# Performance work log

Measured on AMD Instinct MI355X. Metric: run time of the kernel, lower is better.

## Reference

```python
import jax, jax.numpy as jnp
import numpy as np

B, LD, LP, DIM = 8, 128, 1000, 128
LN_EPS = 1e-5


def layer_norm(x, gamma, beta, eps=LN_EPS):
    mu = jnp.mean(x, axis=-1, keepdims=True)
    var = jnp.mean(jnp.square(x - mu), axis=-1, keepdims=True)
    return (x - mu) * jax.lax.rsqrt(var + eps) * gamma + beta


def setup_inputs() -> dict:
    key = jax.random.key(0)
    ks = jax.random.split(key, 8)
    s = 1.0 / np.sqrt(DIM)
    return {
        "drug_conv": jax.random.normal(ks[0], (B, LD, DIM), dtype=jnp.float32),
        "protein_conv": jax.random.normal(ks[1], (B, LP, DIM), dtype=jnp.float32),
        "W_d": jax.random.normal(ks[2], (DIM, DIM), dtype=jnp.float32) * s,
        "b_d": jnp.zeros((DIM,), dtype=jnp.float32),
        "W_p": jax.random.normal(ks[3], (DIM, DIM), dtype=jnp.float32) * s,
        "b_p": jnp.zeros((DIM,), dtype=jnp.float32),
        "W_att": jax.random.normal(ks[4], (DIM, DIM), dtype=jnp.float32) * s,
        "b_att": jnp.zeros((DIM,), dtype=jnp.float32),
        "gamma1": jnp.ones((DIM,), dtype=jnp.float32),
        "beta1": jnp.zeros((DIM,), dtype=jnp.float32),
        "gamma2": jnp.ones((DIM,), dtype=jnp.float32),
        "beta2": jnp.zeros((DIM,), dtype=jnp.float32),
    }


def reference(drug_conv, protein_conv, W_d, b_d, W_p, b_p, W_att, b_att,
              gamma1, beta1, gamma2, beta2):
    # drug_conv: (B, LD, DIM), protein_conv: (B, LP, DIM)
    d_att = drug_conv @ W_d.T + b_d        # (B, LD, DIM)
    p_att = protein_conv @ W_p.T + b_p     # (B, LP, DIM)
    # Pairwise additive interaction (B, LD, LP, DIM) -- the fusable hotspot.
    M = jax.nn.relu(d_att[:, :, None, :] + p_att[:, None, :, :])
    # Linear commutes with mean: apply attention_layer after reduction.
    compound_att = jax.nn.sigmoid(jnp.mean(M, axis=2) @ W_att.T + b_att)  # (B, LD, DIM)
    protein_att = jax.nn.sigmoid(jnp.mean(M, axis=1) @ W_att.T + b_att)   # (B, LP, DIM)
    drug = drug_conv * 0.5 + drug_conv * compound_att
    prot = protein_conv * 0.5 + protein_conv * protein_att
    # MaxPool1d over full length axis == max over L, then LayerNorm(dim).
    drug_vec = layer_norm(jnp.max(drug, axis=1), gamma1, beta1)   # (B, DIM)
    prot_vec = layer_norm(jnp.max(prot, axis=1), gamma2, beta2)   # (B, DIM)
    return (drug_vec, prot_vec)
```

## Files before the change

kernel.cpp:

```cpp
#include <hip/hip_runtime.h>
#include <math.h>

#define B 8
#define LD 128
#define LP 1000
#define LP_PAD 1008
#define DIM 128
#define R 8
#define LN_EPS 1e-5f

#define NBLK_D (B * LD / R)
#define NBLK_P (B * LP / R)
#define SEG_D (NBLK_D / B)
#define SEG_P (NBLK_P / B)

__global__ __launch_bounds__(DIM) void gemv_both(
        const float* __restrict__ Xd, const float* __restrict__ Xp,
        const float* __restrict__ Wd, const float* __restrict__ bd,
        const float* __restrict__ Wp, const float* __restrict__ bp,
        float* __restrict__ outd, float* __restrict__ outp) {
    const int blk = blockIdx.x;
    const int t = threadIdx.x;

    const float *X, *W, *bias;
    float* out;
    int row0;
    if (blk < NBLK_D) { X = Xd; W = Wd; bias = bd; out = outd; row0 = blk * R; }
    else              { X = Xp; W = Wp; bias = bp; out = outp; row0 = (blk - NBLK_D) * R; }

    __shared__ float4 xs4[R][DIM / 4];
    {
        const float4* Xv = reinterpret_cast<const float4*>(X + (size_t)row0 * DIM);
        float4* s = (float4*)xs4;
        s[t] = Xv[t];
        s[t + DIM] = Xv[t + DIM];
    }
    __syncthreads();

    float acc[R];
    const float bv = bias[t];
#pragma unroll
    for (int r = 0; r < R; ++r) acc[r] = bv;

    const float4* w4 = reinterpret_cast<const float4*>(W + t * DIM);
#pragma unroll
    for (int k = 0; k < DIM / 4; ++k) {
        const float4 w = w4[k];
#pragma unroll
        for (int r = 0; r < R; ++r) {
            const float4 x = xs4[r][k];
            acc[r] += w.x * x.x + w.y * x.y + w.z * x.z + w.w * x.w;
        }
    }
#pragma unroll
    for (int r = 0; r < R; ++r) out[(row0 + r) * DIM + t] = acc[r];
}

__global__ __launch_bounds__(256) void pairwise(
        const float* __restrict__ d_att, const float* __restrict__ p_att,
        float* __restrict__ Mc, float* __restrict__ Mp) {
    const int blk = blockIdx.x;
    const int b = blk >> 7;
    const int d = blk & (DIM - 1);
    const int t = threadIdx.x;

    __shared__ float xs[LD];
    __shared__ float2 ys2[LP_PAD / 2];
    __shared__ float red[LD * 8];

    if (t < LD) xs[t] = d_att[(b * LD + t) * DIM + d];
    for (int j = t; j < LP_PAD; j += 256) {
        ((float*)ys2)[j] = (j < LP) ? p_att[(b * LP + j) * DIM + d] : -1e30f;
    }
    __syncthreads();

    for (int p = t; p < LP_PAD / 2; p += 256) {
        const float2 y = ys2[p];
        float2 acc = make_float2(0.f, 0.f);
#pragma unroll 8
        for (int i = 0; i < LD; ++i) {
            const float x = xs[i];
            acc.x += fmaxf(0.f, x + y.x);
            acc.y += fmaxf(0.f, x + y.y);
        }
        const int j = 2 * p;
        if (j < LP)     Mp[(b * LP + j) * DIM + d]     = acc.x * (1.f / (float)LD);
        if (j + 1 < LP) Mp[(b * LP + j + 1) * DIM + d] = acc.y * (1.f / (float)LD);
    }

    {
        const int rq = t >> 3;
        const int sl = t & 7;
        const float x0 = xs[4 * rq + 0];
        const float x1 = xs[4 * rq + 1];
        const float x2 = xs[4 * rq + 2];
        const float x3 = xs[4 * rq + 3];
        float2 a0 = make_float2(0.f, 0.f), a1 = a0, a2 = a0, a3 = a0;
        for (int p = sl; p < LP_PAD / 2; p += 8) {
            const float2 y = ys2[p];
            a0.x += fmaxf(0.f, x0 + y.x); a0.y += fmaxf(0.f, x0 + y.y);
            a1.x += fmaxf(0.f, x1 + y.x); a1.y += fmaxf(0.f, x1 + y.y);
            a2.x += fmaxf(0.f, x2 + y.x); a2.y += fmaxf(0.f, x2 + y.y);
            a3.x += fmaxf(0.f, x3 + y.x); a3.y += fmaxf(0.f, x3 + y.y);
        }
        red[(4 * rq + 0) * 8 + sl] = a0.x + a0.y;
        red[(4 * rq + 1) * 8 + sl] = a1.x + a1.y;
        red[(4 * rq + 2) * 8 + sl] = a2.x + a2.y;
        red[(4 * rq + 3) * 8 + sl] = a3.x + a3.y;
    }
    __syncthreads();
    if (t < LD) {
        float s = 0.f;
#pragma unroll
        for (int k = 0; k < 8; ++k) s += red[t * 8 + k];
        Mc[(b * LD + t) * DIM + d] = s * (1.f / (float)LP);
    }
}

__global__ __launch_bounds__(DIM) void gated_both(
        const float* __restrict__ Mc, const float* __restrict__ Mp,
        const float* __restrict__ W, const float* __restrict__ bias,
        const float* __restrict__ convd, const float* __restrict__ convp,
        float* __restrict__ pd, float* __restrict__ pp) {
    const int blk = blockIdx.x;
    const int t = threadIdx.x;

    const float *M, *conv;
    float* part;
    int row0;
    if (blk < NBLK_D) { M = Mc; conv = convd; part = pd + blk * DIM; row0 = blk * R; }
    else { const int pb = blk - NBLK_D; M = Mp; conv = convp; part = pp + pb * DIM; row0 = pb * R; }

    __shared__ float4 xs4[R][DIM / 4];
    {
        const float4* Mv = reinterpret_cast<const float4*>(M + (size_t)row0 * DIM);
        float4* s = (float4*)xs4;
        s[t] = Mv[t];
        s[t + DIM] = Mv[t + DIM];
    }
    __syncthreads();

    float acc[R];
    const float bv = bias[t];
#pragma unroll
    for (int r = 0; r < R; ++r) acc[r] = bv;

    const float4* w4 = reinterpret_cast<const float4*>(W + t * DIM);
#pragma unroll
    for (int k = 0; k < DIM / 4; ++k) {
        const float4 w = w4[k];
#pragma unroll
        for (int r = 0; r < R; ++r) {
            const float4 x = xs4[r][k];
            acc[r] += w.x * x.x + w.y * x.y + w.z * x.z + w.w * x.w;
        }
    }

    float m = -INFINITY;
#pragma unroll
    for (int r = 0; r < R; ++r) {
        const float att = 1.f / (1.f + expf(-acc[r]));
        const float v = conv[(row0 + r) * DIM + t] * (0.5f + att);
        m = fmaxf(m, v);
    }
    part[t] = m;
}

__global__ __launch_bounds__(256) void maxln_final(
        const float* __restrict__ pd, const float* __restrict__ pp,
        const float* __restrict__ gamma1, const float* __restrict__ beta1,
        const float* __restrict__ gamma2, const float* __restrict__ beta2,
        float* __restrict__ out) {
    const int blk = blockIdx.x;
    const int kind = blk >> 3;
    const int b = blk & 7;
    const int t = threadIdx.x & (DIM - 1);
    const int h = threadIdx.x >> 7;

    float m = -INFINITY;
    if (kind == 0) {
        const float* base = pd + b * SEG_D * DIM;
        for (int s = h; s < SEG_D; s += 2) m = fmaxf(m, base[s * DIM + t]);
    } else {
        const float* base = pp + b * SEG_P * DIM;
        for (int s = h; s < SEG_P; s += 2) m = fmaxf(m, base[s * DIM + t]);
    }

    __shared__ float sm[2][DIM];
    sm[h][t] = m;
    __syncthreads();

    __shared__ float s1[DIM];
    __shared__ float s2[DIM];
    if (threadIdx.x < DIM) {
        m = fmaxf(sm[0][t], sm[1][t]);
        sm[0][t] = m;
        s1[t] = m;
        s2[t] = m * m;
    }
    __syncthreads();
    for (int off = DIM / 2; off > 0; off >>= 1) {
        if (threadIdx.x < off) {
            s1[threadIdx.x] += s1[threadIdx.x + off];
            s2[threadIdx.x] += s2[threadIdx.x + off];
        }
        __syncthreads();
    }
    if (threadIdx.x < DIM) {
        const float mu = s1[0] * (1.f / (float)DIM);
        const float var = s2[0] * (1.f / (float)DIM) - mu * mu;
        const float inv = rsqrtf(var + LN_EPS);
        const float* gamma = kind ? gamma2 : gamma1;
        const float* beta  = kind ? beta2  : beta1;
        const float mv = sm[0][t];
        out[blk * DIM + t] = (mv - mu) * inv * gamma[t] + beta[t];
    }
}

extern "C" void kernel_launch(void* const* d_in, const int* in_sizes, int n_in,
                              void* d_out, int out_size, void* d_ws, size_t ws_size,
                              hipStream_t stream) {
    const float* drug_conv    = (const float*)d_in[0];
    const float* protein_conv = (const float*)d_in[1];
    const float* W_d   = (const float*)d_in[2];
    const float* b_d   = (const float*)d_in[3];
    const float* W_p   = (const float*)d_in[4];
    const float* b_p   = (const float*)d_in[5];
    const float* W_att = (const float*)d_in[6];
    const float* b_att = (const float*)d_in[7];
    const float* gamma1 = (const float*)d_in[8];
    const float* beta1  = (const float*)d_in[9];
    const float* gamma2 = (const float*)d_in[10];
    const float* beta2  = (const float*)d_in[11];
    float* out = (float*)d_out;

    float* ws = (float*)d_ws;
    const size_t n_datt = (size_t)B * LD * DIM;
    const size_t n_patt = (size_t)B * LP * DIM;
    float* d_att = ws;
    float* p_att = ws + n_datt;
    float* Mc    = ws + n_datt + n_patt;
    float* Mp    = ws + n_datt + n_patt + n_datt;
    float* pd = ws;
    float* pp = ws + (size_t)NBLK_D * DIM;

    gemv_both<<<NBLK_D + NBLK_P, DIM, 0, stream>>>(drug_conv, protein_conv,
                                                   W_d, b_d, W_p, b_p, d_att, p_att);
    pairwise<<<B * DIM, 256, 0, stream>>>(d_att, p_att, Mc, Mp);
    gated_both<<<NBLK_D + NBLK_P, DIM, 0, stream>>>(Mc, Mp, W_att, b_att,
                                                    drug_conv, protein_conv, pd, pp);
    maxln_final<<<16, 256, 0, stream>>>(pd, pp, gamma1, beta1, gamma2, beta2, out);
}
```

Before: 145.6 us.

## Use bf16 MFMA for input projections and gated attention linear

Replaces the scalar fp32 GEMV kernels for the drug/protein projections and the attention linear layer with bf16 MFMA 16x16x32 tiles, one wave per 16-row tile. A small kernel converts the three weight matrices to bf16 on each call, and the activation tiles are converted in registers. The gated kernel now does its partial max reduction per tile with lane shuffles and handles the ragged protein tail per batch. This lowers precision to bf16 for these matmuls, which may affect accuracy, and adds an extra launch for the weight conversion.

```diff
diff --git a/kernel.cpp b/kernel.cpp
--- a/kernel.cpp
+++ b/kernel.cpp
@@ -6,54 +6,81 @@
 #define LP 1000
 #define LP_PAD 1008
 #define DIM 128
-#define R 8
 #define LN_EPS 1e-5f
 
-#define NBLK_D (B * LD / R)
-#define NBLK_P (B * LP / R)
-#define SEG_D (NBLK_D / B)
-#define SEG_P (NBLK_P / B)
-
-__global__ __launch_bounds__(DIM) void gemv_both(
+#define TILES_D (B * LD / 16)
+#define TILES_P (B * LP / 16)
+#define GTILES_D 64
+#define GTILES_PB 63
+#define GTILES_P (8 * GTILES_PB)
+#define SEG_D 8
+#define SEG_P GTILES_PB
+
+typedef __attribute__((ext_vector_type(8))) short bf16x8;
+typedef __attribute__((ext_vector_type(4))) float f32x4;
+
+__device__ inline short f2bf(float f) {
+    union { float f; unsigned u; } v; v.f = f;
+    unsigned r = v.u + 0x7fffu + ((v.u >> 16) & 1u);
+    return (short)(r >> 16);
+}
+
+__device__ inline bf16x8 cvt8(float4 lo, float4 hi) {
+    bf16x8 r;
+    r[0] = f2bf(lo.x); r[1] = f2bf(lo.y); r[2] = f2bf(lo.z); r[3] = f2bf(lo.w);
+    r[4] = f2bf(hi.x); r[5] = f2bf(hi.y); r[6] = f2bf(hi.z); r[7] = f2bf(hi.w);
+    return r;
+}
+
+__global__ __launch_bounds__(256) void conv_w(const float* __restrict__ W0,
+                                              const float* __restrict__ W1,
+                                              const float* __restrict__ W2,
+                                              short* __restrict__ out) {
+    const int idx = blockIdx.x * 256 + threadIdx.x;
+    const float* src = idx < 16384 ? W0 : (idx < 32768 ? W1 : W2);
+    out[idx] = f2bf(src[idx & 16383]);
+}
+
+__global__ __launch_bounds__(256) void mfma_gemv(
         const float* __restrict__ Xd, const float* __restrict__ Xp,
-        const float* __restrict__ Wd, const float* __restrict__ bd,
-        const float* __restrict__ Wp, const float* __restrict__ bp,
+        const short* __restrict__ Wdb, const float* __restrict__ bd,
+        const short* __restrict__ Wpb, const float* __restrict__ bp,
         float* __restrict__ outd, float* __restrict__ outp) {
-    const int blk = blockIdx.x;
-    const int t = threadIdx.x;
-
-    const float *X, *W, *bias;
-    float* out;
-    int row0;
-    if (blk < NBLK_D) { X = Xd; W = Wd; bias = bd; out = outd; row0 = blk * R; }
-    else              { X = Xp; W = Wp; bias = bp; out = outp; row0 = (blk - NBLK_D) * R; }
-
-    __shared__ float4 xs4[R][DIM / 4];
+    const int wave = (blockIdx.x * 256 + threadIdx.x) >> 6;
+    const int lane = threadIdx.x & 63;
+
+    const float* X; const short* Wb; const float* bias; float* out; int m0;
+    if (wave < TILES_D) { X = Xd; Wb = Wdb; bias = bd; out = outd; m0 = wave * 16; }
+    else { X = Xp; Wb = Wpb; bias = bp; out = outp; m0 = (wave - TILES_D) * 16; }
+
+    const int arow = lane & 15;
+    const int kgrp = lane >> 4;
+
+    bf16x8 afrag[4];
     {
-        const float4* Xv = reinterpret_cast<const float4*>(X + (size_t)row0 * DIM);
-        float4* s = (float4*)xs4;
-        s[t] = Xv[t];
-        s[t + DIM] = Xv[t + DIM];
-    }
-    __syncthreads();
-
-    float acc[R];
-    const float bv = bias[t];
-#pragma unroll
-    for (int r = 0; r < R; ++r) acc[r] = bv;
-
-    const float4* w4 = reinterpret_cast<const float4*>(W + t * DIM);
-#pragma unroll
-    for (int k = 0; k < DIM / 4; ++k) {
-        const float4 w = w4[k];
-#pragma unroll
-        for (int r = 0; r < R; ++r) {
-            const float4 x = xs4[r][k];
-            acc[r] += w.x * x.x + w.y * x.y + w.z * x.z + w.w * x.w;
-        }
-    }
-#pragma unroll
-    for (int r = 0; r < R; ++r) out[(row0 + r) * DIM + t] = acc[r];
+        const float* xrow = X + (size_t)(m0 + arow) * DIM + kgrp * 8;
+#pragma unroll
+        for (int kk = 0; kk < 4; ++kk)
+            afrag[kk] = cvt8(*(const float4*)(xrow + kk * 32),
+                             *(const float4*)(xrow + kk * 32 + 4));
+    }
+
+    const int ocol = lane & 15;
+    const int orow = (lane >> 4) * 4;
+#pragma unroll
+    for (int nt = 0; nt < 8; ++nt) {
+        const short* wrow = Wb + (size_t)(nt * 16 + arow) * DIM + kgrp * 8;
+        f32x4 c = {0.f, 0.f, 0.f, 0.f};
+#pragma unroll
+        for (int kk = 0; kk < 4; ++kk) {
+            const bf16x8 bfrag = *(const bf16x8*)(wrow + kk * 32);
+            c = __builtin_amdgcn_mfma_f32_16x16x32_bf16(afrag[kk], bfrag, c, 0, 0, 0);
+        }
+        const float bv = bias[nt * 16 + ocol];
+#pragma unroll
+        for (int r = 0; r < 4; ++r)
+            out[(size_t)(m0 + orow + r) * DIM + nt * 16 + ocol] = c[r] + bv;
+    }
 }
 
 __global__ __launch_bounds__(256) void pairwise(
@@ -117,53 +144,70 @@
     }
 }
 
-__global__ __launch_bounds__(DIM) void gated_both(
+__global__ __launch_bounds__(256) void mfma_gated(
         const float* __restrict__ Mc, const float* __restrict__ Mp,
-        const float* __restrict__ W, const float* __restrict__ bias,
+        const short* __restrict__ Wb, const float* __restrict__ bias,
         const float* __restrict__ convd, const float* __restrict__ convp,
         float* __restrict__ pd, float* __restrict__ pp) {
-    const int blk = blockIdx.x;
-    const int t = threadIdx.x;
-
-    const float *M, *conv;
-    float* part;
-    int row0;
-    if (blk < NBLK_D) { M = Mc; conv = convd; part = pd + blk * DIM; row0 = blk * R; }
-    else { const int pb = blk - NBLK_D; M = Mp; conv = convp; part = pp + pb * DIM; row0 = pb * R; }
-
-    __shared__ float4 xs4[R][DIM / 4];
-    {
-        const float4* Mv = reinterpret_cast<const float4*>(M + (size_t)row0 * DIM);
-        float4* s = (float4*)xs4;
-        s[t] = Mv[t];
-        s[t + DIM] = Mv[t + DIM];
-    }
-    __syncthreads();
-
-    float acc[R];
-    const float bv = bias[t];
-#pragma unroll
-    for (int r = 0; r < R; ++r) acc[r] = bv;
-
-    const float4* w4 = reinterpret_cast<const float4*>(W + t * DIM);
-#pragma unroll
-    for (int k = 0; k < DIM / 4; ++k) {
-        const float4 w = w4[k];
-#pragma unroll
-        for (int r = 0; r < R; ++r) {
-            const float4 x = xs4[r][k];
-            acc[r] += w.x * x.x + w.y * x.y + w.z * x.z + w.w * x.w;
-        }
-    }
-
-    float m = -INFINITY;
-#pragma unroll
-    for (int r = 0; r < R; ++r) {
-        const float att = 1.f / (1.f + expf(-acc[r]));
-        const float v = conv[(row0 + r) * DIM + t] * (0.5f + att);
-        m = fmaxf(m, v);
-    }
-    part[t] = m;
+    const int wave = (blockIdx.x * 256 + threadIdx.x) >> 6;
+    const int lane = threadIdx.x & 63;
+
+    const float* M; const float* conv; float* part; int m0; int valid;
+    if (wave < GTILES_D) {
+        M = Mc; conv = convd; part = pd + wave * DIM; m0 = wave * 16; valid = 16;
+    } else {
+        const int pb = wave - GTILES_D;
+        const int b = pb / GTILES_PB;
+        const int s = pb - b * GTILES_PB;
+        M = Mp; conv = convp; part = pp + pb * DIM;
+        m0 = b * LP + s * 16;
+        valid = (s * 16 + 16 <= LP) ? 16 : (LP - s * 16);
+    }
+
+    const int arow = lane & 15;
+    const int kgrp = lane >> 4;
+
+    bf16x8 afrag[4];
+    if (arow < valid) {
+        const float* mrow = M + (size_t)(m0 + arow) * DIM + kgrp * 8;
+#pragma unroll
+        for (int kk = 0; kk < 4; ++kk)
+            afrag[kk] = cvt8(*(const float4*)(mrow + kk * 32),
+                             *(const float4*)(mrow + kk * 32 + 4));
+    } else {
+        bf16x8 z;
+#pragma unroll
+        for (int j = 0; j < 8; ++j) z[j] = 0;
+#pragma unroll
+        for (int kk = 0; kk < 4; ++kk) afrag[kk] = z;
+    }
+
+    const int ocol = lane & 15;
+    const int orow = (lane >> 4) * 4;
+#pragma unroll
+    for (int nt = 0; nt < 8; ++nt) {
+        const short* wrow = Wb + (size_t)(nt * 16 + arow) * DIM + kgrp * 8;
+        f32x4 c = {0.f, 0.f, 0.f, 0.f};
+#pragma unroll
+        for (int kk = 0; kk < 4; ++kk) {
+            const bf16x8 bfrag = *(const bf16x8*)(wrow + kk * 32);
+            c = __builtin_amdgcn_mfma_f32_16x16x32_bf16(afrag[kk], bfrag, c, 0, 0, 0);
+        }
+        const float bv = bias[nt * 16 + ocol];
+        float m = -INFINITY;
+#pragma unroll
+        for (int r = 0; r < 4; ++r) {
+            const int rr = orow + r;
+            if (rr < valid) {
+                const float att = 1.f / (1.f + __expf(-(c[r] + bv)));
+                const float v = conv[(size_t)(m0 + rr) * DIM + nt * 16 + ocol] * (0.5f + att);
+                m = fmaxf(m, v);
+            }
+        }
+        m = fmaxf(m, __shfl_xor(m, 16));
+        m = fmaxf(m, __shfl_xor(m, 32));
+        if (lane < 16) part[nt * 16 + lane] = m;
+    }
 }
 
 __global__ __launch_bounds__(256) void maxln_final(
@@ -212,8 +256,7 @@
         const float inv = rsqrtf(var + LN_EPS);
         const float* gamma = kind ? gamma2 : gamma1;
         const float* beta  = kind ? beta2  : beta1;
-        const float mv = sm[0][t];
-        out[blk * DIM + t] = (mv - mu) * inv * gamma[t] + beta[t];
+        out[blk * DIM + t] = (sm[0][t] - mu) * inv * gamma[t] + beta[t];
     }
 }
 
@@ -241,13 +284,18 @@
     float* p_att = ws + n_datt;
     float* Mc    = ws + n_datt + n_patt;
     float* Mp    = ws + n_datt + n_patt + n_datt;
+    short* wbf   = (short*)(ws + 2310144);
+    short* wb_d   = wbf;
+    short* wb_p   = wbf + 16384;
+    short* wb_att = wbf + 32768;
     float* pd = ws;
-    float* pp = ws + (size_t)NBLK_D * DIM;
-
-    gemv_both<<<NBLK_D + NBLK_P, DIM, 0, stream>>>(drug_conv, protein_conv,
-                                                   W_d, b_d, W_p, b_p, d_att, p_att);
+    float* pp = ws + GTILES_D * DIM;
+
+    conv_w<<<192, 256, 0, stream>>>(W_d, W_p, W_att, wbf);
+    mfma_gemv<<<(TILES_D + TILES_P) / 4, 256, 0, stream>>>(
+        drug_conv, protein_conv, wb_d, b_d, wb_p, b_p, d_att, p_att);
     pairwise<<<B * DIM, 256, 0, stream>>>(d_att, p_att, Mc, Mp);
-    gated_both<<<NBLK_D + NBLK_P, DIM, 0, stream>>>(Mc, Mp, W_att, b_att,
-                                                    drug_conv, protein_conv, pd, pp);
+    mfma_gated<<<(GTILES_D + GTILES_P) / 4, 256, 0, stream>>>(
+        Mc, Mp, wb_att, b_att, drug_conv, protein_conv, pd, pp);
     maxln_final<<<16, 256, 0, stream>>>(pd, pp, gamma1, beta1, gamma2, beta2, out);
 }
```

Result: faster. 140.2 us (-3.7%).
